# Kernel optimization log

Hardware: AMD Instinct MI355X
Metric: run time of the kernel (lower is better)

## Reference

```python
import jax, jax.numpy as jnp
import numpy as np

TOPK = 0.1   # effective steady-state topk (target_topk)
TAU = 0.0    # topk_tau default: pure sparse output


def setup_inputs() -> dict:
    key = jax.random.key(0)
    x = jax.random.normal(key, (64, 256, 64, 64), dtype=jnp.float32)
    return {"x": x}


def reference(x):
    # sparse_hw: keep top-k |value| positions over the H*W axis per (n, c) row.
    n, c, h, w = x.shape
    hw = h * w
    k = int(max(1, TOPK * hw))  # 409 for 64x64 at topk=0.1
    xr = x.reshape(n, c, hw)
    # torch.topk(x_reshape.abs(), k, dim=2) -> indices of k largest magnitudes
    _, idx = jax.lax.top_k(jnp.abs(xr), k)  # idx: [n, c, k]
    # mask = zeros.scatter_(2, idx, 1)
    mask = jnp.zeros_like(xr).at[
        jnp.arange(n)[:, None, None],
        jnp.arange(c)[None, :, None],
        idx,
    ].set(1.0)
    sparse_x = (mask * xr).reshape(n, c, h, w)
    if TAU == 0.0:
        return sparse_x
    # tau blend: tau * x + (1 - tau) * sparse_x
    return TAU * x + (1.0 - TAU) * sparse_x
```

## Files before the change

kernel.cpp:

```cpp
#include <hip/hip_runtime.h>

#define HW_ 4096
#define KSEL 409
#define T0BITS 0x3FC00000u

template<int NBINS>
__device__ __forceinline__ void radix_scan(const unsigned* hist, volatile unsigned* sb,
                                           unsigned kneed, int t) {
  constexpr int C = NBINS / 256;
  unsigned hsum[C];
  #pragma unroll
  for (int q = 0; q < C / 4; ++q) {
    uint4 u = *(const uint4*)&hist[C * t + 4 * q];
    hsum[4*q+0] = u.x; hsum[4*q+1] = u.y; hsum[4*q+2] = u.z; hsum[4*q+3] = u.w;
  }
  unsigned val = 0;
  #pragma unroll
  for (int j = 0; j < C; ++j) val += hsum[j];
  const int lane = t & 63, w = t >> 6;
  unsigned inc = val;
  #pragma unroll
  for (int off = 1; off < 64; off <<= 1) {
    unsigned u = __shfl_down(inc, off);
    if (lane + off < 64) inc += u;
  }
  if (lane == 0) sb[4 + w] = inc;
  __syncthreads();
  unsigned above_waves = 0;
  #pragma unroll
  for (int w2 = 0; w2 < 4; ++w2) if (w2 > w) above_waves += sb[4 + w2];
  const unsigned P = inc + above_waves;
  unsigned cum = P - val;
  if (cum < kneed && kneed <= P) {
    #pragma unroll
    for (int j = C - 1; j >= 0; --j) {
      unsigned h = hsum[j];
      if (cum + h >= kneed) { sb[0] = C * t + j; sb[1] = kneed - cum; sb[2] = h; break; }
      cum += h;
    }
  }
  __syncthreads();
}

extern "C" __global__ void __launch_bounds__(256, 5)
topk_kern(const float* __restrict__ x, float* __restrict__ out) {
  __shared__ unsigned h1[2048];
  __shared__ unsigned h2[1024];
  __shared__ unsigned h3[1024];
  __shared__ unsigned sb[8];
  const int t = threadIdx.x;
  const int lane = t & 63, w = t >> 6;
  const size_t rowoff = (size_t)blockIdx.x * HW_;
  const float4* xr = (const float4*)(x + rowoff);
  float4* orow = (float4*)(out + rowoff);

  float4 v[4];
  unsigned ab[16];
  #pragma unroll
  for (int j = 0; j < 4; ++j) {
    v[j] = xr[t + j * 256];
    ab[4*j+0] = __float_as_uint(v[j].x) & 0x7FFFFFFFu;
    ab[4*j+1] = __float_as_uint(v[j].y) & 0x7FFFFFFFu;
    ab[4*j+2] = __float_as_uint(v[j].z) & 0x7FFFFFFFu;
    ab[4*j+3] = __float_as_uint(v[j].w) & 0x7FFFFFFFu;
  }

  *(uint4*)&h1[4 * t] = make_uint4(0, 0, 0, 0);
  *(uint4*)&h1[4 * t + 1024] = make_uint4(0, 0, 0, 0);
  *(uint4*)&h2[4 * t] = make_uint4(0, 0, 0, 0);
  *(uint4*)&h3[4 * t] = make_uint4(0, 0, 0, 0);
  unsigned cnt = 0;
  #pragma unroll
  for (int i = 0; i < 16; ++i) cnt += (ab[i] > T0BITS) ? 1u : 0u;
  #pragma unroll
  for (int off = 1; off < 64; off <<= 1) cnt += __shfl_down(cnt, off);
  if (lane == 0) sb[4 + w] = cnt;
  __syncthreads();
  const unsigned c0 = sb[4] + sb[5] + sb[6] + sb[7];
  const bool filt = (c0 >= KSEL);

  #pragma unroll
  for (int i = 0; i < 16; ++i)
    if (!filt || ab[i] > T0BITS) atomicAdd(&h1[ab[i] >> 20], 1u);
  __syncthreads();
  radix_scan<2048>(h1, sb, KSEL, t);
  const unsigned b1 = sb[0];
  const unsigned k2 = sb[1];

  #pragma unroll
  for (int i = 0; i < 16; ++i)
    if ((ab[i] >> 20) == b1) atomicAdd(&h2[(ab[i] >> 10) & 0x3FFu], 1u);
  __syncthreads();
  radix_scan<1024>(h2, sb, k2, t);
  const unsigned b2 = sb[0];
  const unsigned k3 = sb[1];
  const unsigned P21 = (b1 << 10) | b2;

  #pragma unroll
  for (int i = 0; i < 16; ++i)
    if ((ab[i] >> 10) == P21) atomicAdd(&h3[ab[i] & 0x3FFu], 1u);
  __syncthreads();
  radix_scan<1024>(h3, sb, k3, t);
  const unsigned b3 = sb[0];
  const unsigned rem = sb[1];
  const unsigned ceq = sb[2];
  const unsigned T = (P21 << 10) | b3;

  unsigned keep = 0;
  #pragma unroll
  for (int i = 0; i < 16; ++i) if (ab[i] > T) keep |= (1u << i);

  if (rem == ceq) {
    #pragma unroll
    for (int i = 0; i < 16; ++i) if (ab[i] == T) keep |= (1u << i);
  } else {
    __syncthreads();
    unsigned* eqh = h1;
    #pragma unroll
    for (int j = 0; j < 4; ++j) {
      unsigned c = 0;
      #pragma unroll
      for (int e = 0; e < 4; ++e) if (ab[4*j+e] == T) ++c;
      eqh[j * 256 + t] = c;
    }
    __syncthreads();
    if (t == 0) {
      unsigned run = 0;
      for (int i = 0; i < 1024; ++i) { unsigned h = eqh[i]; eqh[i] = run; run += h; }
    }
    __syncthreads();
    #pragma unroll
    for (int j = 0; j < 4; ++j) {
      unsigned r = eqh[j * 256 + t];
      #pragma unroll
      for (int e = 0; e < 4; ++e) {
        if (ab[4*j+e] == T) { if (r < rem) keep |= (1u << (4*j + e)); ++r; }
      }
    }
  }

  #pragma unroll
  for (int j = 0; j < 4; ++j) {
    float4 o;
    o.x = ((keep >> (4*j+0)) & 1u) ? v[j].x : 0.0f;
    o.y = ((keep >> (4*j+1)) & 1u) ? v[j].y : 0.0f;
    o.z = ((keep >> (4*j+2)) & 1u) ? v[j].z : 0.0f;
    o.w = ((keep >> (4*j+3)) & 1u) ? v[j].w : 0.0f;
    orow[t + j * 256] = o;
  }
}

extern "C" void kernel_launch(void* const* d_in, const int* in_sizes, int n_in,
                              void* d_out, int out_size, void* d_ws, size_t ws_size,
                              hipStream_t stream) {
  const float* x = (const float*)d_in[0];
  float* out = (float*)d_out;
  const int rows = in_sizes[0] / HW_;
  topk_kern<<<dim3(rows), dim3(256), 0, stream>>>(x, out);
}
```

Before: 428.0 us.

## Process one row per wavefront instead of per block, removing block barriers

Each 64-lane wavefront now handles a whole 4096-element row, with a private 2048-bin LDS histogram per wave and four rows per block. Radix scans use wave-level shuffles and ballot instead of __syncthreads with shared scratch, and the tie-break prefix scan becomes a wave shuffle scan instead of a serial single-thread loop. The goal is to remove block-wide synchronisation overhead. The cost is 64 registers of row data per lane, 32KB LDS per block, and lower occupancy (launch bounds 4), plus more atomic contention per wave histogram.

```diff
diff --git a/kernel.cpp b/kernel.cpp
--- a/kernel.cpp
+++ b/kernel.cpp
@@ -4,149 +4,168 @@
 #define KSEL 409
 #define T0BITS 0x3FC00000u
 
+__device__ __forceinline__ unsigned absbits(unsigned u) { return u & 0x7FFFFFFFu; }
+
 template<int NBINS>
-__device__ __forceinline__ void radix_scan(const unsigned* hist, volatile unsigned* sb,
-                                           unsigned kneed, int t) {
-  constexpr int C = NBINS / 256;
-  unsigned hsum[C];
+__device__ __forceinline__ void wave_scan(const unsigned* hist, unsigned kneed, int lane,
+                                          unsigned& bin, unsigned& rem, unsigned& ceq) {
+  constexpr int C = NBINS / 64;
+  unsigned hs[C];
   #pragma unroll
   for (int q = 0; q < C / 4; ++q) {
-    uint4 u = *(const uint4*)&hist[C * t + 4 * q];
-    hsum[4*q+0] = u.x; hsum[4*q+1] = u.y; hsum[4*q+2] = u.z; hsum[4*q+3] = u.w;
+    uint4 u = *(const uint4*)&hist[C * lane + 4 * q];
+    hs[4*q+0] = u.x; hs[4*q+1] = u.y; hs[4*q+2] = u.z; hs[4*q+3] = u.w;
   }
   unsigned val = 0;
   #pragma unroll
-  for (int j = 0; j < C; ++j) val += hsum[j];
-  const int lane = t & 63, w = t >> 6;
+  for (int j = 0; j < C; ++j) val += hs[j];
   unsigned inc = val;
   #pragma unroll
   for (int off = 1; off < 64; off <<= 1) {
     unsigned u = __shfl_down(inc, off);
     if (lane + off < 64) inc += u;
   }
-  if (lane == 0) sb[4 + w] = inc;
-  __syncthreads();
-  unsigned above_waves = 0;
+  unsigned long long m = __ballot(inc >= kneed);
+  int cl = 63 - __builtin_clzll(m);
+  unsigned bin_c = 0, rem_c = 0, ceq_c = 0, cum = inc - val;
+  bool found = false;
   #pragma unroll
-  for (int w2 = 0; w2 < 4; ++w2) if (w2 > w) above_waves += sb[4 + w2];
-  const unsigned P = inc + above_waves;
-  unsigned cum = P - val;
-  if (cum < kneed && kneed <= P) {
-    #pragma unroll
-    for (int j = C - 1; j >= 0; --j) {
-      unsigned h = hsum[j];
-      if (cum + h >= kneed) { sb[0] = C * t + j; sb[1] = kneed - cum; sb[2] = h; break; }
-      cum += h;
+  for (int j = C - 1; j >= 0; --j) {
+    unsigned h = hs[j];
+    if (!found && cum + h >= kneed) {
+      bin_c = C * lane + j; rem_c = kneed - cum; ceq_c = h; found = true;
     }
+    if (!found) cum += h;
   }
-  __syncthreads();
+  bin = __shfl(bin_c, cl);
+  rem = __shfl(rem_c, cl);
+  ceq = __shfl(ceq_c, cl);
 }
 
-extern "C" __global__ void __launch_bounds__(256, 5)
-topk_kern(const float* __restrict__ x, float* __restrict__ out) {
-  __shared__ unsigned h1[2048];
-  __shared__ unsigned h2[1024];
-  __shared__ unsigned h3[1024];
-  __shared__ unsigned sb[8];
-  const int t = threadIdx.x;
-  const int lane = t & 63, w = t >> 6;
-  const size_t rowoff = (size_t)blockIdx.x * HW_;
-  const float4* xr = (const float4*)(x + rowoff);
-  float4* orow = (float4*)(out + rowoff);
+extern "C" __global__ void __launch_bounds__(256, 4)
+topk_wave(const float* __restrict__ x, float* __restrict__ out) {
+  __shared__ unsigned histall[4][2048];
+  const int lane = threadIdx.x & 63;
+  const int wv = threadIdx.x >> 6;
+  unsigned* hist = histall[wv];
+  const size_t row = (size_t)blockIdx.x * 4 + wv;
+  const uint4* xr = (const uint4*)(x + row * HW_);
+  uint4* orow = (uint4*)(out + row * HW_);
 
-  float4 v[4];
-  unsigned ab[16];
+  uint4 v[16];
   #pragma unroll
-  for (int j = 0; j < 4; ++j) {
-    v[j] = xr[t + j * 256];
-    ab[4*j+0] = __float_as_uint(v[j].x) & 0x7FFFFFFFu;
-    ab[4*j+1] = __float_as_uint(v[j].y) & 0x7FFFFFFFu;
-    ab[4*j+2] = __float_as_uint(v[j].z) & 0x7FFFFFFFu;
-    ab[4*j+3] = __float_as_uint(v[j].w) & 0x7FFFFFFFu;
-  }
+  for (int j = 0; j < 16; ++j) v[j] = xr[lane + 64 * j];
 
-  *(uint4*)&h1[4 * t] = make_uint4(0, 0, 0, 0);
-  *(uint4*)&h1[4 * t + 1024] = make_uint4(0, 0, 0, 0);
-  *(uint4*)&h2[4 * t] = make_uint4(0, 0, 0, 0);
-  *(uint4*)&h3[4 * t] = make_uint4(0, 0, 0, 0);
+  #pragma unroll
+  for (int q = 0; q < 8; ++q)
+    *(uint4*)&hist[32 * lane + 4 * q] = make_uint4(0, 0, 0, 0);
+
   unsigned cnt = 0;
   #pragma unroll
-  for (int i = 0; i < 16; ++i) cnt += (ab[i] > T0BITS) ? 1u : 0u;
+  for (int j = 0; j < 16; ++j) {
+    cnt += (absbits(v[j].x) > T0BITS);
+    cnt += (absbits(v[j].y) > T0BITS);
+    cnt += (absbits(v[j].z) > T0BITS);
+    cnt += (absbits(v[j].w) > T0BITS);
+  }
+  unsigned red = cnt;
   #pragma unroll
-  for (int off = 1; off < 64; off <<= 1) cnt += __shfl_down(cnt, off);
-  if (lane == 0) sb[4 + w] = cnt;
-  __syncthreads();
-  const unsigned c0 = sb[4] + sb[5] + sb[6] + sb[7];
+  for (int off = 1; off < 64; off <<= 1) red += __shfl_down(red, off);
+  const unsigned c0 = __shfl(red, 0);
   const bool filt = (c0 >= KSEL);
 
   #pragma unroll
-  for (int i = 0; i < 16; ++i)
-    if (!filt || ab[i] > T0BITS) atomicAdd(&h1[ab[i] >> 20], 1u);
-  __syncthreads();
-  radix_scan<2048>(h1, sb, KSEL, t);
-  const unsigned b1 = sb[0];
-  const unsigned k2 = sb[1];
+  for (int j = 0; j < 16; ++j) {
+    unsigned a;
+    a = absbits(v[j].x); if (!filt || a > T0BITS) atomicAdd(&hist[a >> 20], 1u);
+    a = absbits(v[j].y); if (!filt || a > T0BITS) atomicAdd(&hist[a >> 20], 1u);
+    a = absbits(v[j].z); if (!filt || a > T0BITS) atomicAdd(&hist[a >> 20], 1u);
+    a = absbits(v[j].w); if (!filt || a > T0BITS) atomicAdd(&hist[a >> 20], 1u);
+  }
+  unsigned b1, k2, ceq1;
+  wave_scan<2048>(hist, KSEL, lane, b1, k2, ceq1);
 
   #pragma unroll
-  for (int i = 0; i < 16; ++i)
-    if ((ab[i] >> 20) == b1) atomicAdd(&h2[(ab[i] >> 10) & 0x3FFu], 1u);
-  __syncthreads();
-  radix_scan<1024>(h2, sb, k2, t);
-  const unsigned b2 = sb[0];
-  const unsigned k3 = sb[1];
+  for (int q = 0; q < 4; ++q)
+    *(uint4*)&hist[16 * lane + 4 * q] = make_uint4(0, 0, 0, 0);
+  #pragma unroll
+  for (int j = 0; j < 16; ++j) {
+    unsigned a;
+    a = absbits(v[j].x); if ((a >> 20) == b1) atomicAdd(&hist[(a >> 10) & 0x3FFu], 1u);
+    a = absbits(v[j].y); if ((a >> 20) == b1) atomicAdd(&hist[(a >> 10) & 0x3FFu], 1u);
+    a = absbits(v[j].z); if ((a >> 20) == b1) atomicAdd(&hist[(a >> 10) & 0x3FFu], 1u);
+    a = absbits(v[j].w); if ((a >> 20) == b1) atomicAdd(&hist[(a >> 10) & 0x3FFu], 1u);
+  }
+  unsigned b2, k3, ceq2;
+  wave_scan<1024>(hist, k2, lane, b2, k3, ceq2);
   const unsigned P21 = (b1 << 10) | b2;
 
   #pragma unroll
-  for (int i = 0; i < 16; ++i)
-    if ((ab[i] >> 10) == P21) atomicAdd(&h3[ab[i] & 0x3FFu], 1u);
-  __syncthreads();
-  radix_scan<1024>(h3, sb, k3, t);
-  const unsigned b3 = sb[0];
-  const unsigned rem = sb[1];
-  const unsigned ceq = sb[2];
+  for (int q = 0; q < 4; ++q)
+    *(uint4*)&hist[16 * lane + 4 * q] = make_uint4(0, 0, 0, 0);
+  #pragma unroll
+  for (int j = 0; j < 16; ++j) {
+    unsigned a;
+    a = absbits(v[j].x); if ((a >> 10) == P21) atomicAdd(&hist[a & 0x3FFu], 1u);
+    a = absbits(v[j].y); if ((a >> 10) == P21) atomicAdd(&hist[a & 0x3FFu], 1u);
+    a = absbits(v[j].z); if ((a >> 10) == P21) atomicAdd(&hist[a & 0x3FFu], 1u);
+    a = absbits(v[j].w); if ((a >> 10) == P21) atomicAdd(&hist[a & 0x3FFu], 1u);
+  }
+  unsigned b3, rem, ceq;
+  wave_scan<1024>(hist, k3, lane, b3, rem, ceq);
   const unsigned T = (P21 << 10) | b3;
 
-  unsigned keep = 0;
+  unsigned long long keep = 0;
   #pragma unroll
-  for (int i = 0; i < 16; ++i) if (ab[i] > T) keep |= (1u << i);
+  for (int j = 0; j < 16; ++j) {
+    if (absbits(v[j].x) > T) keep |= (1ull << (4*j+0));
+    if (absbits(v[j].y) > T) keep |= (1ull << (4*j+1));
+    if (absbits(v[j].z) > T) keep |= (1ull << (4*j+2));
+    if (absbits(v[j].w) > T) keep |= (1ull << (4*j+3));
+  }
 
   if (rem == ceq) {
     #pragma unroll
-    for (int i = 0; i < 16; ++i) if (ab[i] == T) keep |= (1u << i);
+    for (int j = 0; j < 16; ++j) {
+      if (absbits(v[j].x) == T) keep |= (1ull << (4*j+0));
+      if (absbits(v[j].y) == T) keep |= (1ull << (4*j+1));
+      if (absbits(v[j].z) == T) keep |= (1ull << (4*j+2));
+      if (absbits(v[j].w) == T) keep |= (1ull << (4*j+3));
+    }
   } else {
-    __syncthreads();
-    unsigned* eqh = h1;
+    unsigned base = 0;
     #pragma unroll
-    for (int j = 0; j < 4; ++j) {
-      unsigned c = 0;
+    for (int j = 0; j < 16; ++j) {
+      unsigned eqm = 0;
+      if (absbits(v[j].x) == T) eqm |= 1u;
+      if (absbits(v[j].y) == T) eqm |= 2u;
+      if (absbits(v[j].z) == T) eqm |= 4u;
+      if (absbits(v[j].w) == T) eqm |= 8u;
+      unsigned c = __popc(eqm);
+      unsigned inc2 = c;
       #pragma unroll
-      for (int e = 0; e < 4; ++e) if (ab[4*j+e] == T) ++c;
-      eqh[j * 256 + t] = c;
-    }
-    __syncthreads();
-    if (t == 0) {
-      unsigned run = 0;
-      for (int i = 0; i < 1024; ++i) { unsigned h = eqh[i]; eqh[i] = run; run += h; }
-    }
-    __syncthreads();
-    #pragma unroll
-    for (int j = 0; j < 4; ++j) {
-      unsigned r = eqh[j * 256 + t];
+      for (int off = 1; off < 64; off <<= 1) {
+        unsigned u = __shfl_up(inc2, off);
+        if (lane >= off) inc2 += u;
+      }
+      unsigned r = base + inc2 - c;
+      unsigned tot = __shfl(inc2, 63);
       #pragma unroll
       for (int e = 0; e < 4; ++e) {
-        if (ab[4*j+e] == T) { if (r < rem) keep |= (1u << (4*j + e)); ++r; }
+        if ((eqm >> e) & 1u) { if (r < rem) keep |= (1ull << (4*j+e)); ++r; }
       }
+      base += tot;
     }
   }
 
   #pragma unroll
-  for (int j = 0; j < 4; ++j) {
-    float4 o;
-    o.x = ((keep >> (4*j+0)) & 1u) ? v[j].x : 0.0f;
-    o.y = ((keep >> (4*j+1)) & 1u) ? v[j].y : 0.0f;
-    o.z = ((keep >> (4*j+2)) & 1u) ? v[j].z : 0.0f;
-    o.w = ((keep >> (4*j+3)) & 1u) ? v[j].w : 0.0f;
-    orow[t + j * 256] = o;
+  for (int j = 0; j < 16; ++j) {
+    uint4 o;
+    o.x = ((keep >> (4*j+0)) & 1ull) ? v[j].x : 0u;
+    o.y = ((keep >> (4*j+1)) & 1ull) ? v[j].y : 0u;
+    o.z = ((keep >> (4*j+2)) & 1ull) ? v[j].z : 0u;
+    o.w = ((keep >> (4*j+3)) & 1ull) ? v[j].w : 0u;
+    orow[lane + 64 * j] = o;
   }
 }
 
@@ -156,5 +175,5 @@
   const float* x = (const float*)d_in[0];
   float* out = (float*)d_out;
   const int rows = in_sizes[0] / HW_;
-  topk_kern<<<dim3(rows), dim3(256), 0, stream>>>(x, out);
+  topk_wave<<<dim3(rows / 4), dim3(256), 0, stream>>>(x, out);
 }
```

New measurement: 489.1 us. +14.3%, slower.
